# Kernel tuning notes

Hardware: AMD Instinct MI355X
Metric: run time of the kernel (lower is better)

## Reference

```python
import jax, jax.numpy as jnp
import numpy as np
import math

EMBED = 1024
FF = 4096
B, S = 4, 2048
EPS = 1e-5


def setup_inputs() -> dict:
    key = jax.random.key(0)
    ks = jax.random.split(key, 12)
    sd = 1.0 / math.sqrt(EMBED)
    inp = {
        "x": jax.random.normal(ks[0], (B, S, EMBED), dtype=jnp.float32),
        "Wq": jax.random.normal(ks[1], (EMBED, EMBED), dtype=jnp.float32) * sd,
        "bq": jnp.zeros((EMBED,), jnp.float32),
        "Wk": jax.random.normal(ks[2], (EMBED, EMBED), dtype=jnp.float32) * sd,
        "bk": jnp.zeros((EMBED,), jnp.float32),
        "Wv": jax.random.normal(ks[3], (EMBED, EMBED), dtype=jnp.float32) * sd,
        "bv": jnp.zeros((EMBED,), jnp.float32),
        "W1": jax.random.normal(ks[4], (EMBED, FF), dtype=jnp.float32) * sd,
        "b1": jnp.zeros((FF,), jnp.float32),
        "W2": jax.random.normal(ks[5], (FF, EMBED), dtype=jnp.float32) * (1.0 / math.sqrt(FF)),
        "b2": jnp.zeros((EMBED,), jnp.float32),
        "g1": jnp.ones((EMBED,), jnp.float32),
        "be1": jnp.zeros((EMBED,), jnp.float32),
        "g2": jnp.ones((EMBED,), jnp.float32),
        "be2": jnp.zeros((EMBED,), jnp.float32),
    }
    return inp


def _sinusoidal_pe(seq_len, d):
    pos = jnp.arange(seq_len, dtype=jnp.float32)[:, None]          # [S,1]
    div = jnp.exp(jnp.arange(0, d, 2, dtype=jnp.float32) * (-math.log(10000.0) / d))
    pe = jnp.zeros((seq_len, d), jnp.float32)
    pe = pe.at[:, 0::2].set(jnp.sin(pos * div))
    pe = pe.at[:, 1::2].set(jnp.cos(pos * div))
    return pe  # [S,d]


def _layernorm(x, g, b):
    mu = jnp.mean(x, axis=-1, keepdims=True)
    var = jnp.mean(jnp.square(x - mu), axis=-1, keepdims=True)
    return (x - mu) * jax.lax.rsqrt(var + EPS) * g + b


def reference(x, Wq, bq, Wk, bk, Wv, bv, W1, b1, W2, b2, g1, be1, g2, be2):
    d = x.shape[-1]
    x = x + _sinusoidal_pe(x.shape[1], d)[None]
    q = x @ Wq + bq
    k = x @ Wk + bk
    v = x @ Wv + bv
    energy = jnp.einsum("bqd,bkd->bqk", q, k) / math.sqrt(d)
    attn = jax.nn.softmax(energy, axis=-1)
    attn_out = jnp.einsum("bqk,bkd->bqd", attn, v)
    h = _layernorm(attn_out + x, g1, be1)
    ff = jax.nn.relu(h @ W1 + b1) @ W2 + b2
    return _layernorm(ff + h, g2, be2)
```

## Files before the change

kernel.cpp:

```cpp
#include <hip/hip_runtime.h>
#include <hip/hip_bf16.h>
#include <cmath>
#include <cstdint>

typedef __bf16 bf16;
typedef __bf16 bf16x8 __attribute__((ext_vector_type(8)));
typedef __bf16 bf16x4 __attribute__((ext_vector_type(4)));
typedef float  f32x4  __attribute__((ext_vector_type(4)));

#define EMBED 1024
#define FFDIM 4096
#define BATCH 4
#define SEQ   2048
#define MTOK  (BATCH*SEQ)

static constexpr size_t OFF_HB    = 0;
static constexpr size_t OFF_XPE_B = 32ull << 20;
static constexpr size_t OFF_Q     = 48ull << 20;
static constexpr size_t OFF_K     = 64ull << 20;
static constexpr size_t OFF_VT    = 80ull << 20;
static constexpr size_t OFF_E     = 96ull << 20;
static constexpr size_t OFF_ATTN  = 160ull << 20;
static constexpr size_t OFF_WQKVT = 224ull << 20;
static constexpr size_t OFF_W1T   = 230ull << 20;
static constexpr size_t OFF_W2T   = 238ull << 20;

#define VMCNT4 { asm volatile("s_waitcnt vmcnt(4)" ::: "memory"); __builtin_amdgcn_sched_barrier(0); }
#define VMCNT0 { asm volatile("s_waitcnt vmcnt(0)" ::: "memory"); __builtin_amdgcn_sched_barrier(0); }
#define PH_BAR  { __builtin_amdgcn_sched_barrier(0); __builtin_amdgcn_s_barrier(); \
                  asm volatile("s_waitcnt lgkmcnt(0)" ::: "memory"); __builtin_amdgcn_sched_barrier(0); }
#define PH_END  { __builtin_amdgcn_sched_barrier(0); }
#define BARONLY { __builtin_amdgcn_sched_barrier(0); __builtin_amdgcn_s_barrier(); \
                  __builtin_amdgcn_sched_barrier(0); }

__device__ __forceinline__ void gload_lds16(const void* g, void* l) {
  __builtin_amdgcn_global_load_lds((const __attribute__((address_space(1))) void*)g,
                                   (__attribute__((address_space(3))) void*)l, 16, 0, 0);
}

__global__ __launch_bounds__(256) void pe_add_kernel(const float* __restrict__ x,
                                                     bf16* __restrict__ xb) {
  int idx  = blockIdx.x * 256 + threadIdx.x;
  int pair = idx & 511;
  int s    = idx >> 9;
  float div = __expf((float)(2 * pair) * (-9.210340371976184f / (float)EMBED));
  float ang = (float)s * div;
  float sv = sinf(ang), cv = cosf(ang);
#pragma unroll
  for (int b = 0; b < BATCH; ++b) {
    size_t base = ((size_t)(b * SEQ + s)) * EMBED + (size_t)pair * 2;
    xb[base]     = (bf16)(x[base] + sv);
    xb[base + 1] = (bf16)(x[base + 1] + cv);
  }
}

__global__ __launch_bounds__(256) void transpose_kernel(const float* __restrict__ W,
                                                        bf16* __restrict__ Wt,
                                                        int K, int N) {
  __shared__ float tile[32][33];
  int nb = blockIdx.x * 32, kb = blockIdx.y * 32;
  int tx = threadIdx.x, ty = threadIdx.y;
#pragma unroll
  for (int i = 0; i < 32; i += 8)
    tile[ty + i][tx] = W[(size_t)(kb + ty + i) * N + nb + tx];
  __syncthreads();
#pragma unroll
  for (int i = 0; i < 32; i += 8)
    Wt[(size_t)(nb + ty + i) * K + kb + tx] = (bf16)tile[tx][ty + i];
}

__global__ __launch_bounds__(256) void vtrans_kernel(const bf16* __restrict__ V,
                                                     bf16* __restrict__ VT) {
  __shared__ ushort tile[32][36];
  const int d0 = blockIdx.x * 32, s0 = blockIdx.y * 32, b = blockIdx.z;
  const ushort* src = (const ushort*)V + ((size_t)b * SEQ + s0) * EMBED + d0;
  ushort* dst = (ushort*)VT + ((size_t)b * EMBED + d0) * SEQ + s0;
  const int tx = threadIdx.x, ty = threadIdx.y;
#pragma unroll
  for (int i = 0; i < 32; i += 8)
    tile[ty + i][tx] = src[(size_t)(ty + i) * EMBED + tx];
  __syncthreads();
#pragma unroll
  for (int i = 0; i < 32; i += 8)
    dst[(size_t)(ty + i) * SEQ + tx] = tile[tx][ty + i];
}

#define BMX 256
#define BNX 256
#define BKX 64

#define MM16(QR, QC, FB) { \
  __builtin_amdgcn_s_setprio(1); \
  _Pragma("unroll") for (int kk = 0; kk < 2; ++kk) \
  _Pragma("unroll") for (int i2 = 0; i2 < 4; ++i2) \
  _Pragma("unroll") for (int j2 = 0; j2 < 2; ++j2) \
    acc[(QR)*4 + i2][(QC)*2 + j2] = __builtin_amdgcn_mfma_f32_16x16x32_bf16( \
        fa[kk][i2], FB[kk][j2], acc[(QR)*4 + i2][(QC)*2 + j2], 0, 0, 0); \
  __builtin_amdgcn_s_setprio(0); }

template <int EPI>
__global__ __launch_bounds__(512, 2) void gemm8_kernel(
    const bf16* __restrict__ A, const bf16* __restrict__ B,
    const float* __restrict__ bias, void* __restrict__ out,
    int K, int lda, int ldb, int ldo, int NB,
    long long sAz, long long sBz, long long sOz,
    long long sAk, long long sBk, long long sOk,
    float scale,
    const float* bias2, const float* bias3, void* out2, void* out3) {
  __shared__ __align__(16) char ldsA[2 * 32768];
  __shared__ __align__(16) char ldsB[2 * 32768];

  const int gx = gridDim.x, gy = gridDim.y;
  int id = blockIdx.x + gx * (blockIdx.y + gy * blockIdx.z);
  const int nwg = gx * gy * gridDim.z;
  const int qd = nwg >> 3, rm = nwg & 7;
  const int xcd = id & 7, pos = id >> 3;
  const int lid = (xcd < rm ? xcd * (qd + 1) : rm * (qd + 1) + (xcd - rm) * qd) + pos;
  const int per = gx * gy;
  const int tz = lid / per;
  const int s2 = lid - tz * per;
  const int G = 8;
  const int ngrp = G * gy;
  const int grp = s2 / ngrp;
  const int within = s2 - grp * ngrp;
  const int gwf = gx - grp * G;
  const int gw = gwf < G ? gwf : G;
  const int tx = grp * G + within % gw;
  const int ty = within / gw;

  const int zb = tz % NB;
  const int kh = tz / NB;
  A += (long long)zb * sAz + (long long)kh * sAk;
  B += (long long)zb * sBz + (long long)kh * sBk;

  const int tid  = threadIdx.x;
  const int wave = tid >> 6;
  const int lane = tid & 63;
  const int wm = wave >> 2, wn = wave & 3;
  const int rowBase = ty * BMX;
  const int colBase = tx * BNX;
  const int lr = lane & 15;
  const int g  = lane >> 4;
  const int lx = lr & 7;

  const int rr = tid >> 3;
  const int slot = (tid & 7) ^ (rr & 7);
  const bf16* Abase = A + (long long)(rowBase + rr) * lda + slot * 8;
  const bf16* Bb0 = B + (long long)(colBase + (rr & 31) + ((rr >> 5)) * 64) * ldb + slot * 8;
  const bf16* Bb1 = B + (long long)(colBase + (rr & 31) + (2 + (rr >> 5)) * 64) * ldb + slot * 8;

  auto stA = [&](int T, int bufOff, int qr) {
    char* dst = ldsA + bufOff + qr * 16384 + wave * 1024;
    const bf16* s = Abase + (long long)(qr * 64) * lda + (long long)T * BKX;
    gload_lds16(s, dst);
    gload_lds16(s + (long long)128 * lda, dst + 8192);
  };
  auto stB = [&](int T, int bufOff, int qc) {
    char* dst = ldsB + bufOff + qc * 16384 + wave * 1024;
    const long long off = (long long)(qc * 32) * ldb + (long long)T * BKX;
    gload_lds16(Bb0 + off, dst);
    gload_lds16(Bb1 + off, dst + 8192);
  };

  bf16x8 fa[2][4], fbq0[2][2], fbq1[2][2];
  auto rdFA = [&](int bufOff, int qr) {
    const char* base = ldsA + bufOff + qr * 16384 + wm * 8192;
#pragma unroll
    for (int kk = 0; kk < 2; ++kk) {
      const int sw = ((kk * 4 + g) ^ lx) << 4;
#pragma unroll
      for (int i2 = 0; i2 < 4; ++i2)
        fa[kk][i2] = *(const bf16x8*)(base + (i2 * 16 + lr) * 128 + sw);
    }
  };
  auto rdFB = [&](int bufOff, int qc, bf16x8 fb[2][2]) {
    const char* base = ldsB + bufOff + qc * 16384 + wn * 4096;
#pragma unroll
    for (int kk = 0; kk < 2; ++kk) {
      const int sw = ((kk * 4 + g) ^ lx) << 4;
#pragma unroll
      for (int j2 = 0; j2 < 2; ++j2)
        fb[kk][j2] = *(const bf16x8*)(base + (j2 * 16 + lr) * 128 + sw);
    }
  };

  const f32x4 zero4 = {0.f, 0.f, 0.f, 0.f};
  f32x4 acc[8][4];
#pragma unroll
  for (int i = 0; i < 8; ++i)
#pragma unroll
    for (int j = 0; j < 4; ++j) acc[i][j] = zero4;

  const int nK = K / BKX;

  stA(0, 0, 0); stB(0, 0, 0); stA(0, 0, 1); stB(0, 0, 1);
  stA(1, 32768, 0); stB(1, 32768, 0);
  VMCNT4;
  __builtin_amdgcn_s_barrier(); __builtin_amdgcn_sched_barrier(0);

#define STEP(STG) { \
    rdFA(0, 0); rdFB(0, 0, fbq0); stA(T0 + 1, 32768, 1);               \
    PH_BAR; MM16(0, 0, fbq0); PH_END; \
    rdFB(0, 1, fbq1); stB(T0 + 1, 32768, 1);                           \
    PH_BAR; MM16(0, 1, fbq1); PH_END; \
    rdFA(0, 1); if (STG) stA(T0 + 2, 0, 0);                            \
    PH_BAR; MM16(1, 0, fbq0); PH_END; \
    if (STG) stB(T0 + 2, 0, 0);                                        \
    MM16(1, 1, fbq1); \
    if (STG) { VMCNT4 } else { VMCNT0 } \
    BARONLY; \
    rdFA(32768, 0); rdFB(32768, 0, fbq0); if (STG) stA(T0 + 2, 0, 1);  \
    PH_BAR; MM16(0, 0, fbq0); PH_END; \
    rdFB(32768, 1, fbq1); if (STG) stB(T0 + 2, 0, 1);                  \
    PH_BAR; MM16(0, 1, fbq1); PH_END; \
    rdFA(32768, 1); if (STG) stA(T0 + 3, 32768, 0);                    \
    PH_BAR; MM16(1, 0, fbq0); PH_END; \
    if (STG) stB(T0 + 3, 32768, 0);                                    \
    MM16(1, 1, fbq1); \
    if (STG) { VMCNT4 } \
    BARONLY; \
  }

  int T0 = 0;
  for (; T0 + 2 < nK; T0 += 2) STEP(1);
  STEP(0);
#undef STEP

#pragma unroll
  for (int j = 0; j < 4; ++j) {
    const int col = colBase + wn * 64 + (j >> 1) * 32 + (j & 1) * 16 + lr;
#pragma unroll
    for (int i = 0; i < 8; ++i) {
      const int row0 = rowBase + wm * 128 + (i >> 2) * 64 + (i & 3) * 16 + g * 4;
      if constexpr (EPI == 6) {
        const int cb = col >> 10;
        const int c  = col & 1023;
        const float bv = (cb == 0 ? bias : (cb == 1 ? bias2 : bias3))[c];
        bf16* dst = (cb == 0 ? (bf16*)out : (cb == 1 ? (bf16*)out2 : (bf16*)out3));
#pragma unroll
        for (int rr2 = 0; rr2 < 4; ++rr2)
          dst[(size_t)(row0 + rr2) * EMBED + c] = (bf16)(acc[i][j][rr2] + bv);
      } else if constexpr (EPI == 2) {
        float* dst = (float*)out + (long long)zb * sOz + (long long)kh * sOk;
#pragma unroll
        for (int rr2 = 0; rr2 < 4; ++rr2)
          dst[(long long)(row0 + rr2) * ldo + col] = acc[i][j][rr2] * scale;
      } else if constexpr (EPI == 5) {
        bf16* dst = (bf16*)out + (long long)zb * sOz;
#pragma unroll
        for (int rr2 = 0; rr2 < 4; ++rr2)
          dst[(long long)(row0 + rr2) * ldo + col] = (bf16)(acc[i][j][rr2] * scale);
      } else if constexpr (EPI == 3) {
        const float bv = bias[col];
#pragma unroll
        for (int rr2 = 0; rr2 < 4; ++rr2) {
          float t = acc[i][j][rr2] + bv;
          ((bf16*)out)[(size_t)(row0 + rr2) * ldo + col] = (bf16)(t > 0.f ? t : 0.f);
        }
      }
    }
  }
}

__global__ __launch_bounds__(256) void softmax_kernel(const bf16* __restrict__ E,
                                                      bf16* __restrict__ P) {
  const size_t row = blockIdx.x;
  const int t = threadIdx.x;
  bf16x8 ev = *(const bf16x8*)(E + row * SEQ + (size_t)t * 8);
  float e[8];
#pragma unroll
  for (int q = 0; q < 8; ++q) e[q] = (float)ev[q];
  float m = e[0];
#pragma unroll
  for (int q = 1; q < 8; ++q) m = fmaxf(m, e[q]);
#pragma unroll
  for (int o = 32; o; o >>= 1) m = fmaxf(m, __shfl_xor(m, o));
  __shared__ float red[8];
  const int w = t >> 6;
  if ((t & 63) == 0) red[w] = m;
  __syncthreads();
  m = fmaxf(fmaxf(red[0], red[1]), fmaxf(red[2], red[3]));
  float s = 0.f;
#pragma unroll
  for (int q = 0; q < 8; ++q) { e[q] = __expf(e[q] - m); s += e[q]; }
#pragma unroll
  for (int o = 32; o; o >>= 1) s += __shfl_xor(s, o);
  if ((t & 63) == 0) red[4 + w] = s;
  __syncthreads();
  s = red[4] + red[5] + red[6] + red[7];
  const float inv = 1.0f / s;
  bf16x8 pv;
#pragma unroll
  for (int q = 0; q < 8; ++q) pv[q] = (bf16)(e[q] * inv);
  *(bf16x8*)(P + row * SEQ + (size_t)t * 8) = pv;
}

__global__ __launch_bounds__(256) void ln_kernel(const float* __restrict__ X,
                                                 const float* __restrict__ X2,
                                                 const bf16* __restrict__ Rb,
                                                 const float* __restrict__ cb,
                                                 const float* __restrict__ gm,
                                                 const float* __restrict__ bt,
                                                 float* __restrict__ of,
                                                 bf16* __restrict__ ob) {
  const size_t row = blockIdx.x;
  const int t = threadIdx.x;
  float4 xv = ((const float4*)(X + row * EMBED))[t];
  bf16x4 rv = *(const bf16x4*)(Rb + row * EMBED + (size_t)t * 4);
  float4 v;
  v.x = xv.x + (float)rv[0]; v.y = xv.y + (float)rv[1];
  v.z = xv.z + (float)rv[2]; v.w = xv.w + (float)rv[3];
  if (X2) {
    float4 x2 = ((const float4*)(X2 + row * EMBED))[t];
    v.x += x2.x; v.y += x2.y; v.z += x2.z; v.w += x2.w;
  }
  if (cb) {
    float4 c4 = ((const float4*)cb)[t];
    v.x += c4.x; v.y += c4.y; v.z += c4.z; v.w += c4.w;
  }
  float s  = v.x + v.y + v.z + v.w;
  float ss = v.x * v.x + v.y * v.y + v.z * v.z + v.w * v.w;
#pragma unroll
  for (int o = 32; o; o >>= 1) { s += __shfl_xor(s, o); ss += __shfl_xor(ss, o); }
  __shared__ float red[8];
  const int w = t >> 6;
  if ((t & 63) == 0) { red[w] = s; red[4 + w] = ss; }
  __syncthreads();
  s  = red[0] + red[1] + red[2] + red[3];
  ss = red[4] + red[5] + red[6] + red[7];
  const float mu  = s * (1.0f / EMBED);
  const float inv = rsqrtf(ss * (1.0f / EMBED) - mu * mu + 1e-5f);
  float4 gv = ((const float4*)gm)[t];
  float4 bv = ((const float4*)bt)[t];
  float4 o4;
  o4.x = (v.x - mu) * inv * gv.x + bv.x;
  o4.y = (v.y - mu) * inv * gv.y + bv.y;
  o4.z = (v.z - mu) * inv * gv.z + bv.z;
  o4.w = (v.w - mu) * inv * gv.w + bv.w;
  if (of) ((float4*)(of + row * EMBED))[t] = o4;
  if (ob) {
    bf16x4 p;
    p[0] = (bf16)o4.x; p[1] = (bf16)o4.y; p[2] = (bf16)o4.z; p[3] = (bf16)o4.w;
    *(bf16x4*)(ob + row * EMBED + (size_t)t * 4) = p;
  }
}

extern "C" void kernel_launch(void* const* d_in, const int* in_sizes, int n_in,
                              void* d_out, int out_size, void* d_ws, size_t ws_size,
                              hipStream_t stream) {
  const float* x   = (const float*)d_in[0];
  const float* Wq  = (const float*)d_in[1];
  const float* bq  = (const float*)d_in[2];
  const float* Wk  = (const float*)d_in[3];
  const float* bk  = (const float*)d_in[4];
  const float* Wv  = (const float*)d_in[5];
  const float* bv  = (const float*)d_in[6];
  const float* W1  = (const float*)d_in[7];
  const float* b1  = (const float*)d_in[8];
  const float* W2  = (const float*)d_in[9];
  const float* b2  = (const float*)d_in[10];
  const float* g1  = (const float*)d_in[11];
  const float* be1 = (const float*)d_in[12];
  const float* g2  = (const float*)d_in[13];
  const float* be2 = (const float*)d_in[14];
  float* out = (float*)d_out;
  char* ws = (char*)d_ws;

  bf16*  hb   = (bf16*)(ws + OFF_HB);
  bf16*  xpeb = (bf16*)(ws + OFF_XPE_B);
  bf16*  Qb   = (bf16*)(ws + OFF_Q);
  bf16*  Kb   = (bf16*)(ws + OFF_K);
  bf16*  VT   = (bf16*)(ws + OFF_VT);
  bf16*  Vb   = (bf16*)(ws + OFF_ATTN);
  bf16*  E    = (bf16*)(ws + OFF_E);
  bf16*  P    = (bf16*)(ws + OFF_Q);
  float* pv0  = (float*)(ws + OFF_ATTN);
  float* pv1  = (float*)(ws + OFF_E);
  bf16*  T1   = (bf16*)(ws + OFF_E);
  float* ff0  = (float*)(ws + OFF_ATTN);
  float* ff1  = (float*)(ws + OFF_Q);
  bf16*  WqkvT = (bf16*)(ws + OFF_WQKVT);
  bf16*  W1T  = (bf16*)(ws + OFF_W1T);
  bf16*  W2T  = (bf16*)(ws + OFF_W2T);

  const long long sOk_pv = (long long)(OFF_E / 4) - (long long)(OFF_ATTN / 4);
  const long long sOk_ff = (long long)(OFF_Q / 4) - (long long)(OFF_ATTN / 4);

  const dim3 tb(32, 8);
  transpose_kernel<<<dim3(EMBED / 32, EMBED / 32), tb, 0, stream>>>(Wq, WqkvT, EMBED, EMBED);
  transpose_kernel<<<dim3(EMBED / 32, EMBED / 32), tb, 0, stream>>>(Wk, WqkvT + (size_t)EMBED * EMBED, EMBED, EMBED);
  transpose_kernel<<<dim3(EMBED / 32, EMBED / 32), tb, 0, stream>>>(Wv, WqkvT + 2ull * EMBED * EMBED, EMBED, EMBED);
  transpose_kernel<<<dim3(FFDIM / 32, EMBED / 32), tb, 0, stream>>>(W1, W1T, EMBED, FFDIM);
  transpose_kernel<<<dim3(EMBED / 32, FFDIM / 32), tb, 0, stream>>>(W2, W2T, FFDIM, EMBED);

  pe_add_kernel<<<(SEQ * 512) / 256, 256, 0, stream>>>(x, xpeb);

  gemm8_kernel<6><<<dim3(3072 / BNX, MTOK / BMX, 1), 512, 0, stream>>>(
      xpeb, WqkvT, bq, Qb, EMBED, EMBED, EMBED, EMBED, 1,
      0, 0, 0, 0, 0, 0, 1.0f, bk, bv, Kb, Vb);

  vtrans_kernel<<<dim3(EMBED / 32, SEQ / 32, BATCH), tb, 0, stream>>>(Vb, VT);

  gemm8_kernel<5><<<dim3(SEQ / BNX, SEQ / BMX, BATCH), 512, 0, stream>>>(
      Qb, Kb, nullptr, E, EMBED, EMBED, EMBED, SEQ, BATCH,
      (long long)SEQ * EMBED, (long long)SEQ * EMBED, (long long)SEQ * SEQ,
      0, 0, 0, 0.03125f, nullptr, nullptr, nullptr, nullptr);

  softmax_kernel<<<BATCH * SEQ, 256, 0, stream>>>(E, P);

  gemm8_kernel<2><<<dim3(EMBED / BNX, SEQ / BMX, BATCH * 2), 512, 0, stream>>>(
      P, VT, nullptr, pv0, 1024, SEQ, SEQ, EMBED, BATCH,
      (long long)SEQ * SEQ, (long long)EMBED * SEQ, (long long)SEQ * EMBED,
      1024, 1024, sOk_pv,
      1.0f, nullptr, nullptr, nullptr, nullptr);

  ln_kernel<<<MTOK, 256, 0, stream>>>(pv0, pv1, xpeb, nullptr, g1, be1, nullptr, hb);

  gemm8_kernel<3><<<dim3(FFDIM / BNX, MTOK / BMX, 1), 512, 0, stream>>>(
      hb, W1T, b1, T1, EMBED, EMBED, EMBED, FFDIM, 1,
      0, 0, 0, 0, 0, 0, 1.0f, nullptr, nullptr, nullptr, nullptr);

  gemm8_kernel<2><<<dim3(EMBED / BNX, MTOK / BMX, 2), 512, 0, stream>>>(
      T1, W2T, nullptr, ff0, 2048, FFDIM, FFDIM, EMBED, 1,
      0, 0, 0,
      2048, 2048, sOk_ff,
      1.0f, nullptr, nullptr, nullptr, nullptr);

  ln_kernel<<<MTOK, 256, 0, stream>>>(ff0, ff1, hb, b2, g2, be2, out, nullptr);
}
```

Measured before the change: 375.3 us.

## Store split-K partials in bf16 and relax vmcnt waits in GEMM pipeline

The split-K partial outputs of the PV and FF2 GEMMs are now written as bf16 instead of fp32 through the bf16 epilogue, and the LayerNorm kernels read them as bf16. This halves the partial-sum write and read traffic. Separately, the GEMM main loop's global-load waits change from vmcnt(4) to vmcnt(8) at the stage boundary, with an added vmcnt(6) before the first phase barrier, which allows more loads in flight. The bf16 partials lose precision before the residual add and LayerNorm, and the new wait counts must still match the number of outstanding loads.

```diff
diff --git a/kernel.cpp b/kernel.cpp
--- a/kernel.cpp
+++ b/kernel.cpp
@@ -25,7 +25,8 @@
 static constexpr size_t OFF_W1T   = 230ull << 20;
 static constexpr size_t OFF_W2T   = 238ull << 20;
 
-#define VMCNT4 { asm volatile("s_waitcnt vmcnt(4)" ::: "memory"); __builtin_amdgcn_sched_barrier(0); }
+#define VMCNT6 { asm volatile("s_waitcnt vmcnt(6)" ::: "memory"); __builtin_amdgcn_sched_barrier(0); }
+#define VMCNT8 { asm volatile("s_waitcnt vmcnt(8)" ::: "memory"); __builtin_amdgcn_sched_barrier(0); }
 #define VMCNT0 { asm volatile("s_waitcnt vmcnt(0)" ::: "memory"); __builtin_amdgcn_sched_barrier(0); }
 #define PH_BAR  { __builtin_amdgcn_sched_barrier(0); __builtin_amdgcn_s_barrier(); \
                   asm volatile("s_waitcnt lgkmcnt(0)" ::: "memory"); __builtin_amdgcn_sched_barrier(0); }
@@ -195,29 +196,29 @@
 
   stA(0, 0, 0); stB(0, 0, 0); stA(0, 0, 1); stB(0, 0, 1);
   stA(1, 32768, 0); stB(1, 32768, 0);
-  VMCNT4;
+  { asm volatile("s_waitcnt vmcnt(4)" ::: "memory"); __builtin_amdgcn_sched_barrier(0); }
   __builtin_amdgcn_s_barrier(); __builtin_amdgcn_sched_barrier(0);
 
 #define STEP(STG) { \
     rdFA(0, 0); rdFB(0, 0, fbq0); stA(T0 + 1, 32768, 1);               \
-    PH_BAR; MM16(0, 0, fbq0); PH_END; \
+    VMCNT6; PH_BAR; MM16(0, 0, fbq0); PH_END; \
     rdFB(0, 1, fbq1); stB(T0 + 1, 32768, 1);                           \
     PH_BAR; MM16(0, 1, fbq1); PH_END; \
     rdFA(0, 1); if (STG) stA(T0 + 2, 0, 0);                            \
     PH_BAR; MM16(1, 0, fbq0); PH_END; \
     if (STG) stB(T0 + 2, 0, 0);                                        \
     MM16(1, 1, fbq1); \
-    if (STG) { VMCNT4 } else { VMCNT0 } \
+    if (STG) { VMCNT8 } else { VMCNT0 } \
     BARONLY; \
     rdFA(32768, 0); rdFB(32768, 0, fbq0); if (STG) stA(T0 + 2, 0, 1);  \
-    PH_BAR; MM16(0, 0, fbq0); PH_END; \
+    VMCNT6; PH_BAR; MM16(0, 0, fbq0); PH_END; \
     rdFB(32768, 1, fbq1); if (STG) stB(T0 + 2, 0, 1);                  \
     PH_BAR; MM16(0, 1, fbq1); PH_END; \
     rdFA(32768, 1); if (STG) stA(T0 + 3, 32768, 0);                    \
     PH_BAR; MM16(1, 0, fbq0); PH_END; \
     if (STG) stB(T0 + 3, 32768, 0);                                    \
     MM16(1, 1, fbq1); \
-    if (STG) { VMCNT4 } \
+    if (STG) { VMCNT8 } \
     BARONLY; \
   }
 
@@ -240,13 +241,8 @@
 #pragma unroll
         for (int rr2 = 0; rr2 < 4; ++rr2)
           dst[(size_t)(row0 + rr2) * EMBED + c] = (bf16)(acc[i][j][rr2] + bv);
-      } else if constexpr (EPI == 2) {
-        float* dst = (float*)out + (long long)zb * sOz + (long long)kh * sOk;
-#pragma unroll
-        for (int rr2 = 0; rr2 < 4; ++rr2)
-          dst[(long long)(row0 + rr2) * ldo + col] = acc[i][j][rr2] * scale;
       } else if constexpr (EPI == 5) {
-        bf16* dst = (bf16*)out + (long long)zb * sOz;
+        bf16* dst = (bf16*)out + (long long)zb * sOz + (long long)kh * sOk;
 #pragma unroll
         for (int rr2 = 0; rr2 < 4; ++rr2)
           dst[(long long)(row0 + rr2) * ldo + col] = (bf16)(acc[i][j][rr2] * scale);
@@ -295,8 +291,8 @@
   *(bf16x8*)(P + row * SEQ + (size_t)t * 8) = pv;
 }
 
-__global__ __launch_bounds__(256) void ln_kernel(const float* __restrict__ X,
-                                                 const float* __restrict__ X2,
+__global__ __launch_bounds__(256) void ln_kernel(const bf16* __restrict__ Xb,
+                                                 const bf16* __restrict__ X2b,
                                                  const bf16* __restrict__ Rb,
                                                  const float* __restrict__ cb,
                                                  const float* __restrict__ gm,
@@ -305,14 +301,16 @@
                                                  bf16* __restrict__ ob) {
   const size_t row = blockIdx.x;
   const int t = threadIdx.x;
-  float4 xv = ((const float4*)(X + row * EMBED))[t];
+  bf16x4 xv = *(const bf16x4*)(Xb + row * EMBED + (size_t)t * 4);
   bf16x4 rv = *(const bf16x4*)(Rb + row * EMBED + (size_t)t * 4);
   float4 v;
-  v.x = xv.x + (float)rv[0]; v.y = xv.y + (float)rv[1];
-  v.z = xv.z + (float)rv[2]; v.w = xv.w + (float)rv[3];
-  if (X2) {
-    float4 x2 = ((const float4*)(X2 + row * EMBED))[t];
-    v.x += x2.x; v.y += x2.y; v.z += x2.z; v.w += x2.w;
+  v.x = (float)xv[0] + (float)rv[0];
+  v.y = (float)xv[1] + (float)rv[1];
+  v.z = (float)xv[2] + (float)rv[2];
+  v.w = (float)xv[3] + (float)rv[3];
+  if (X2b) {
+    bf16x4 x2 = *(const bf16x4*)(X2b + row * EMBED + (size_t)t * 4);
+    v.x += (float)x2[0]; v.y += (float)x2[1]; v.z += (float)x2[2]; v.w += (float)x2[3];
   }
   if (cb) {
     float4 c4 = ((const float4*)cb)[t];
@@ -374,17 +372,17 @@
   bf16*  Vb   = (bf16*)(ws + OFF_ATTN);
   bf16*  E    = (bf16*)(ws + OFF_E);
   bf16*  P    = (bf16*)(ws + OFF_Q);
-  float* pv0  = (float*)(ws + OFF_ATTN);
-  float* pv1  = (float*)(ws + OFF_E);
+  bf16*  pv0  = (bf16*)(ws + OFF_ATTN);
+  bf16*  pv1  = (bf16*)(ws + OFF_E);
   bf16*  T1   = (bf16*)(ws + OFF_E);
-  float* ff0  = (float*)(ws + OFF_ATTN);
-  float* ff1  = (float*)(ws + OFF_Q);
+  bf16*  ff0  = (bf16*)(ws + OFF_ATTN);
+  bf16*  ff1  = (bf16*)(ws + OFF_Q);
   bf16*  WqkvT = (bf16*)(ws + OFF_WQKVT);
   bf16*  W1T  = (bf16*)(ws + OFF_W1T);
   bf16*  W2T  = (bf16*)(ws + OFF_W2T);
 
-  const long long sOk_pv = (long long)(OFF_E / 4) - (long long)(OFF_ATTN / 4);
-  const long long sOk_ff = (long long)(OFF_Q / 4) - (long long)(OFF_ATTN / 4);
+  const long long sOk_pv = ((long long)OFF_E - (long long)OFF_ATTN) / 2;
+  const long long sOk_ff = ((long long)OFF_Q - (long long)OFF_ATTN) / 2;
 
   const dim3 tb(32, 8);
   transpose_kernel<<<dim3(EMBED / 32, EMBED / 32), tb, 0, stream>>>(Wq, WqkvT, EMBED, EMBED);
@@ -408,7 +406,7 @@
 
   softmax_kernel<<<BATCH * SEQ, 256, 0, stream>>>(E, P);
 
-  gemm8_kernel<2><<<dim3(EMBED / BNX, SEQ / BMX, BATCH * 2), 512, 0, stream>>>(
+  gemm8_kernel<5><<<dim3(EMBED / BNX, SEQ / BMX, BATCH * 2), 512, 0, stream>>>(
       P, VT, nullptr, pv0, 1024, SEQ, SEQ, EMBED, BATCH,
       (long long)SEQ * SEQ, (long long)EMBED * SEQ, (long long)SEQ * EMBED,
       1024, 1024, sOk_pv,
@@ -420,7 +418,7 @@
       hb, W1T, b1, T1, EMBED, EMBED, EMBED, FFDIM, 1,
       0, 0, 0, 0, 0, 0, 1.0f, nullptr, nullptr, nullptr, nullptr);
 
-  gemm8_kernel<2><<<dim3(EMBED / BNX, MTOK / BMX, 2), 512, 0, stream>>>(
+  gemm8_kernel<5><<<dim3(EMBED / BNX, MTOK / BMX, 2), 512, 0, stream>>>(
       T1, W2T, nullptr, ff0, 2048, FFDIM, FFDIM, EMBED, 1,
       0, 0, 0,
       2048, 2048, sOk_ff,
```

New measurement: 362.2 us. -3.5%, faster.
